# Kernel tuning notes

Measured on AMD Instinct MI355X. Metric: run time of the kernel, lower is better.

## Reference

```python
import jax, jax.numpy as jnp
import numpy as np


def _compute_deltas(ts, m):
    """Affine time-decay recurrence: delta_0 = 0; for t>=1:
    delta_t = gap_t + (1 - m_{t-1}) * delta_{t-1}, with gap broadcast over features.
    ts: [b, s] timestamps, m: [b, s, f] float 0/1 mask. Returns [b, s, f]."""
    b, s, f = m.shape
    gaps = ts[:, 1:] - ts[:, :-1]          # [b, s-1]
    a = 1.0 - m[:, :-1, :]                 # [b, s-1, f] decay coefficient

    def step(d, inp):
        g_t, a_t = inp                      # g_t: [b], a_t: [b, f]
        d = g_t[:, None] + a_t * d
        return d, d

    gT = jnp.swapaxes(gaps, 0, 1)          # [s-1, b]
    aT = jnp.swapaxes(a, 0, 1)             # [s-1, b, f]
    _, ds = jax.lax.scan(step, jnp.zeros((b, f), ts.dtype), (gT, aT))
    ds = jnp.swapaxes(ds, 0, 1)            # [b, s-1, f]
    return jnp.concatenate([jnp.zeros((b, 1, f), ts.dtype), ds], axis=1)


def setup_inputs() -> dict:
    key = jax.random.key(0)
    k1, k2, k3 = jax.random.split(key, 3)
    b, s, f = 32, 2048, 768
    # monotonically increasing timestamps (cumsum of positive gaps)
    gaps = jax.random.uniform(k1, (b, s), minval=1.0, maxval=60.0, dtype=jnp.float32)
    timestamps = jnp.cumsum(gaps, axis=1)
    encoded_data = jax.random.normal(k2, (b, s, f), dtype=jnp.float32)
    masks = jax.random.randint(k3, (b, s, f), 0, 2, dtype=jnp.int32)
    return {"timestamps": timestamps, "encoded_data": encoded_data, "masks": masks}


def reference(timestamps, encoded_data, masks):
    """JAX translation of _prepare_brits_data. Returns stacked
    [forward_deltas, backward_deltas, backward_X] of shape [3, b, s, f].
    (forward X / masks are pass-through inputs; backward mask is flip(masks).)"""
    m = masks.astype(timestamps.dtype)
    forward_deltas = _compute_deltas(timestamps, m)
    ts_b = jnp.flip(timestamps, axis=1)
    m_b = jnp.flip(m, axis=1)
    backward_deltas = jnp.abs(_compute_deltas(ts_b, m_b))
    x_b = jnp.flip(encoded_data, axis=1)
    return jnp.stack([forward_deltas, backward_deltas, x_b], axis=0)
```

## Files before the change

### kernel.cpp

```cpp
#include <hip/hip_runtime.h>
#include <stdint.h>

static constexpr int B = 32, S = 2048, F = 768;
static constexpr int SC = 64;
static constexpr int NSC = S / SC;
static constexpr int F4 = F / 4;
static constexpr int FT = F4;

typedef float v4f __attribute__((ext_vector_type(4)));

__device__ __forceinline__ v4f mk4(float a, float b, float c, float d) {
    v4f v; v.x = a; v.y = b; v.z = c; v.w = d; return v;
}

__global__ __launch_bounds__(FT) void deltaK(const float* __restrict__ ts,
                                             const int4* __restrict__ masks,
                                             float* __restrict__ out) {
    const int pair = blockIdx.x;
    const int b  = pair >> 5;
    const int sc = pair & (NSC - 1);
    const int g0 = sc * SC;
    const int j  = threadIdx.x;
    const size_t N4 = (size_t)B * S * F4;

    const float* tsb = ts + (size_t)b * S;
    const int4* mbase = masks + (size_t)b * S * F4 + j;

    __shared__ float tss[SC];
    if (j < SC) tss[j] = tsb[g0 + j];
    __syncthreads();

    uint32_t a0 = 0, a1 = 0, a2 = 0, a3 = 0;
    uint32_t c0 = 0, c1 = 0, c2 = 0, c3 = 0;
    #pragma unroll
    for (int g = 0; g < 8; ++g) {
        int4 mv[8];
        #pragma unroll
        for (int q = 0; q < 8; ++q) mv[q] = mbase[(size_t)(g0 + g * 8 + q) * F4];
        #pragma unroll
        for (int q = 0; q < 8; ++q) {
            const int k = g * 8 + q;
            const uint32_t bit = 1u << (k & 31);
            if (k < 32) {
                if (mv[q].x) a0 |= bit;
                if (mv[q].y) a1 |= bit;
                if (mv[q].z) a2 |= bit;
                if (mv[q].w) a3 |= bit;
            } else {
                if (mv[q].x) c0 |= bit;
                if (mv[q].y) c1 |= bit;
                if (mv[q].z) c2 |= bit;
                if (mv[q].w) c3 |= bit;
            }
        }
    }

    float t0v = tsb[0];
    float p0 = t0v, p1 = t0v, p2 = t0v, p3 = t0v;
    if (g0 > 0) {
        unsigned um = 0xFu;
        int r = g0 - 1;
        while (um && r >= 0) {
            int rl = (r - 7 > 0) ? r - 7 : 0;
            int nn = r - rl + 1;
            int4 mv[8];
            #pragma unroll
            for (int q = 0; q < 8; ++q) if (q < nn) mv[q] = mbase[(size_t)(r - q) * F4];
            #pragma unroll
            for (int q = 0; q < 8; ++q) if (q < nn) {
                float t = tsb[r - q];
                if ((um & 1u) && mv[q].x) { p0 = t; um &= ~1u; }
                if ((um & 2u) && mv[q].y) { p1 = t; um &= ~2u; }
                if ((um & 4u) && mv[q].z) { p2 = t; um &= ~4u; }
                if ((um & 8u) && mv[q].w) { p3 = t; um &= ~8u; }
            }
            r = rl - 1;
        }
    }

    float tev = tsb[S - 1];
    float n0 = tev, n1 = tev, n2 = tev, n3 = tev;
    if (g0 + SC < S) {
        unsigned um = 0xFu;
        int r = g0 + SC;
        while (um && r < S) {
            int rh = (r + 7 < S - 1) ? r + 7 : S - 1;
            int nn = rh - r + 1;
            int4 mv[8];
            #pragma unroll
            for (int q = 0; q < 8; ++q) if (q < nn) mv[q] = mbase[(size_t)(r + q) * F4];
            #pragma unroll
            for (int q = 0; q < 8; ++q) if (q < nn) {
                float t = tsb[r + q];
                if ((um & 1u) && mv[q].x) { n0 = t; um &= ~1u; }
                if ((um & 2u) && mv[q].y) { n1 = t; um &= ~2u; }
                if ((um & 4u) && mv[q].z) { n2 = t; um &= ~4u; }
                if ((um & 8u) && mv[q].w) { n3 = t; um &= ~8u; }
            }
            r = rh + 1;
        }
    }

    v4f* o0 = reinterpret_cast<v4f*>(out) + (size_t)(b * S + g0) * F4 + j;
    #pragma unroll
    for (int k = 0; k < 32; ++k) {
        float t = tss[k];
        __builtin_nontemporal_store(mk4(t - p0, t - p1, t - p2, t - p3), &o0[(size_t)k * F4]);
        const uint32_t bit = 1u << k;
        if (a0 & bit) p0 = t;
        if (a1 & bit) p1 = t;
        if (a2 & bit) p2 = t;
        if (a3 & bit) p3 = t;
    }
    #pragma unroll
    for (int k = 32; k < 64; ++k) {
        float t = tss[k];
        __builtin_nontemporal_store(mk4(t - p0, t - p1, t - p2, t - p3), &o0[(size_t)k * F4]);
        const uint32_t bit = 1u << (k - 32);
        if (c0 & bit) p0 = t;
        if (c1 & bit) p1 = t;
        if (c2 & bit) p2 = t;
        if (c3 & bit) p3 = t;
    }

    v4f* o1b = reinterpret_cast<v4f*>(out) + N4 + (size_t)b * S * F4 + j;
    #pragma unroll
    for (int k = 63; k >= 32; --k) {
        float t = tss[k];
        size_t fr = (size_t)(S - 1 - g0 - k) * F4;
        __builtin_nontemporal_store(mk4(n0 - t, n1 - t, n2 - t, n3 - t), &o1b[fr]);
        const uint32_t bit = 1u << (k - 32);
        if (c0 & bit) n0 = t;
        if (c1 & bit) n1 = t;
        if (c2 & bit) n2 = t;
        if (c3 & bit) n3 = t;
    }
    #pragma unroll
    for (int k = 31; k >= 0; --k) {
        float t = tss[k];
        size_t fr = (size_t)(S - 1 - g0 - k) * F4;
        __builtin_nontemporal_store(mk4(n0 - t, n1 - t, n2 - t, n3 - t), &o1b[fr]);
        const uint32_t bit = 1u << k;
        if (a0 & bit) n0 = t;
        if (a1 & bit) n1 = t;
        if (a2 & bit) n2 = t;
        if (a3 & bit) n3 = t;
    }
}

static constexpr int CPY_BLOCKS = 2048;
__global__ __launch_bounds__(256) void copyK(const v4f* __restrict__ x,
                                             v4f* __restrict__ o2) {
    const size_t N4 = (size_t)B * S * F4;
    const size_t stride = (size_t)CPY_BLOCKS * 256;
    for (size_t i = (size_t)blockIdx.x * 256 + threadIdx.x; i < N4; i += stride) {
        size_t row = i / F4;
        size_t f   = i - row * F4;
        size_t t   = row & (S - 1);
        size_t src = (row - t + (S - 1 - t)) * F4 + f;
        __builtin_nontemporal_store(__builtin_nontemporal_load(&x[src]), &o2[i]);
    }
}

extern "C" void kernel_launch(void* const* d_in, const int* in_sizes, int n_in,
                              void* d_out, int out_size, void* d_ws, size_t ws_size,
                              hipStream_t stream) {
    const float* ts    = (const float*)d_in[0];
    const v4f* x       = (const v4f*)d_in[1];
    const int4*  masks = (const int4*)d_in[2];
    float* out = (float*)d_out;
    const size_t N4 = (size_t)B * S * F4;
    deltaK<<<B * NSC, FT, 0, stream>>>(ts, masks, out);
    copyK<<<CPY_BLOCKS, 256, 0, stream>>>(x, reinterpret_cast<v4f*>(out) + 2 * N4);
}
```

Baseline: 194.1 us.

## Split delta kernel into bitmask-packing pass and bitmask-based scan pass

The delta kernel is split into two passes. The first reads each 64-row chunk of the mask once, packs it into per-feature 64-bit bitmasks and writes them to workspace. The second finds the previous and next observed timestamps across chunk boundaries by scanning those compact bitmasks with clz/ffs, replacing the re-reads of full int32 mask rows. This adds an extra launch and a workspace round trip; the old fused kernel is kept as a fallback when the workspace is too small.

```diff
diff --git a/kernel.cpp b/kernel.cpp
--- a/kernel.cpp
+++ b/kernel.cpp
@@ -2,41 +2,32 @@
 #include <stdint.h>
 
 static constexpr int B = 32, S = 2048, F = 768;
-static constexpr int SC = 64;
-static constexpr int NSC = S / SC;
+static constexpr int CS = 64;
+static constexpr int NCH = S / CS;
 static constexpr int F4 = F / 4;
 static constexpr int FT = F4;
 
 typedef float v4f __attribute__((ext_vector_type(4)));
+typedef int   v4i __attribute__((ext_vector_type(4)));
+typedef unsigned int v4u __attribute__((ext_vector_type(4)));
 
 __device__ __forceinline__ v4f mk4(float a, float b, float c, float d) {
     v4f v; v.x = a; v.y = b; v.z = c; v.w = d; return v;
 }
 
-__global__ __launch_bounds__(FT) void deltaK(const float* __restrict__ ts,
-                                             const int4* __restrict__ masks,
-                                             float* __restrict__ out) {
-    const int pair = blockIdx.x;
-    const int b  = pair >> 5;
-    const int sc = pair & (NSC - 1);
-    const int g0 = sc * SC;
-    const int j  = threadIdx.x;
-    const size_t N4 = (size_t)B * S * F4;
-
-    const float* tsb = ts + (size_t)b * S;
-    const int4* mbase = masks + (size_t)b * S * F4 + j;
-
-    __shared__ float tss[SC];
-    if (j < SC) tss[j] = tsb[g0 + j];
-    __syncthreads();
-
+__global__ __launch_bounds__(FT) void passA(const v4i* __restrict__ masks,
+                                            uint32_t* __restrict__ bw) {
+    const int blk = blockIdx.x;
+    const int b = blk >> 5, c = blk & 31;
+    const int j = threadIdx.x;
+    const v4i* mp = masks + (size_t)(b * S + c * CS) * F4 + j;
     uint32_t a0 = 0, a1 = 0, a2 = 0, a3 = 0;
     uint32_t c0 = 0, c1 = 0, c2 = 0, c3 = 0;
     #pragma unroll
     for (int g = 0; g < 8; ++g) {
-        int4 mv[8];
-        #pragma unroll
-        for (int q = 0; q < 8; ++q) mv[q] = mbase[(size_t)(g0 + g * 8 + q) * F4];
+        v4i mv[8];
+        #pragma unroll
+        for (int q = 0; q < 8; ++q) mv[q] = __builtin_nontemporal_load(&mp[(size_t)(g * 8 + q) * F4]);
         #pragma unroll
         for (int q = 0; q < 8; ++q) {
             const int k = g * 8 + q;
@@ -54,50 +45,65 @@
             }
         }
     }
-
-    float t0v = tsb[0];
-    float p0 = t0v, p1 = t0v, p2 = t0v, p3 = t0v;
-    if (g0 > 0) {
-        unsigned um = 0xFu;
-        int r = g0 - 1;
-        while (um && r >= 0) {
-            int rl = (r - 7 > 0) ? r - 7 : 0;
-            int nn = r - rl + 1;
-            int4 mv[8];
-            #pragma unroll
-            for (int q = 0; q < 8; ++q) if (q < nn) mv[q] = mbase[(size_t)(r - q) * F4];
-            #pragma unroll
-            for (int q = 0; q < 8; ++q) if (q < nn) {
-                float t = tsb[r - q];
-                if ((um & 1u) && mv[q].x) { p0 = t; um &= ~1u; }
-                if ((um & 2u) && mv[q].y) { p1 = t; um &= ~2u; }
-                if ((um & 4u) && mv[q].z) { p2 = t; um &= ~4u; }
-                if ((um & 8u) && mv[q].w) { p3 = t; um &= ~8u; }
-            }
-            r = rl - 1;
-        }
-    }
-
-    float tev = tsb[S - 1];
-    float n0 = tev, n1 = tev, n2 = tev, n3 = tev;
-    if (g0 + SC < S) {
-        unsigned um = 0xFu;
-        int r = g0 + SC;
-        while (um && r < S) {
-            int rh = (r + 7 < S - 1) ? r + 7 : S - 1;
-            int nn = rh - r + 1;
-            int4 mv[8];
-            #pragma unroll
-            for (int q = 0; q < 8; ++q) if (q < nn) mv[q] = mbase[(size_t)(r + q) * F4];
-            #pragma unroll
-            for (int q = 0; q < 8; ++q) if (q < nn) {
-                float t = tsb[r + q];
-                if ((um & 1u) && mv[q].x) { n0 = t; um &= ~1u; }
-                if ((um & 2u) && mv[q].y) { n1 = t; um &= ~2u; }
-                if ((um & 4u) && mv[q].z) { n2 = t; um &= ~4u; }
-                if ((um & 8u) && mv[q].w) { n3 = t; um &= ~8u; }
-            }
-            r = rh + 1;
+    v4u w0; w0.x = a0; w0.y = c0; w0.z = a1; w0.w = c1;
+    v4u w1; w1.x = a2; w1.y = c2; w1.z = a3; w1.w = c3;
+    v4u* dst = reinterpret_cast<v4u*>(bw + ((size_t)blk * F + 4 * j) * 2);
+    dst[0] = w0;
+    dst[1] = w1;
+}
+
+__global__ __launch_bounds__(FT) void passC(const float* __restrict__ ts,
+                                            const uint32_t* __restrict__ bw,
+                                            float* __restrict__ out) {
+    const int blk = blockIdx.x;
+    const int b = blk >> 5, c = blk & 31;
+    const int g0 = c * CS;
+    const int j = threadIdx.x;
+    const size_t N4 = (size_t)B * S * F4;
+    const float* tsb = ts + (size_t)b * S;
+
+    __shared__ float tss[CS];
+    if (j < CS) tss[j] = tsb[g0 + j];
+    __syncthreads();
+
+    const v4u* own = reinterpret_cast<const v4u*>(bw + ((size_t)blk * F + 4 * j) * 2);
+    v4u w0 = own[0], w1 = own[1];
+    uint32_t alo[4] = {w0.x, w0.z, w1.x, w1.z};
+    uint32_t ahi[4] = {w0.y, w0.w, w1.y, w1.w};
+
+    float p[4], n[4];
+    {
+        float def = tsb[0];
+        p[0] = p[1] = p[2] = p[3] = def;
+        uint32_t need = 0xFu;
+        for (int d = c - 1; d >= 0 && need; --d) {
+            const v4u* nb = reinterpret_cast<const v4u*>(bw + ((size_t)(b * NCH + d) * F + 4 * j) * 2);
+            v4u u0 = nb[0], u1 = nb[1];
+            uint32_t lo[4] = {u0.x, u0.z, u1.x, u1.z};
+            uint32_t hi[4] = {u0.y, u0.w, u1.y, u1.w};
+            const int base = d * CS;
+            #pragma unroll
+            for (int i = 0; i < 4; ++i) if (need & (1u << i)) {
+                if (hi[i])      { p[i] = tsb[base + 32 + (31 - __clz((int)hi[i]))]; need &= ~(1u << i); }
+                else if (lo[i]) { p[i] = tsb[base +      (31 - __clz((int)lo[i]))]; need &= ~(1u << i); }
+            }
+        }
+    }
+    {
+        float def = tsb[S - 1];
+        n[0] = n[1] = n[2] = n[3] = def;
+        uint32_t need = 0xFu;
+        for (int d = c + 1; d < NCH && need; ++d) {
+            const v4u* nb = reinterpret_cast<const v4u*>(bw + ((size_t)(b * NCH + d) * F + 4 * j) * 2);
+            v4u u0 = nb[0], u1 = nb[1];
+            uint32_t lo[4] = {u0.x, u0.z, u1.x, u1.z};
+            uint32_t hi[4] = {u0.y, u0.w, u1.y, u1.w};
+            const int base = d * CS;
+            #pragma unroll
+            for (int i = 0; i < 4; ++i) if (need & (1u << i)) {
+                if (lo[i])      { n[i] = tsb[base +      (__ffs((int)lo[i]) - 1)]; need &= ~(1u << i); }
+                else if (hi[i]) { n[i] = tsb[base + 32 + (__ffs((int)hi[i]) - 1)]; need &= ~(1u << i); }
+            }
         }
     }
 
@@ -105,22 +111,18 @@
     #pragma unroll
     for (int k = 0; k < 32; ++k) {
         float t = tss[k];
-        __builtin_nontemporal_store(mk4(t - p0, t - p1, t - p2, t - p3), &o0[(size_t)k * F4]);
-        const uint32_t bit = 1u << k;
-        if (a0 & bit) p0 = t;
-        if (a1 & bit) p1 = t;
-        if (a2 & bit) p2 = t;
-        if (a3 & bit) p3 = t;
+        __builtin_nontemporal_store(mk4(t - p[0], t - p[1], t - p[2], t - p[3]), &o0[(size_t)k * F4]);
+        const uint32_t bit = 1u << k;
+        #pragma unroll
+        for (int i = 0; i < 4; ++i) if (alo[i] & bit) p[i] = t;
     }
     #pragma unroll
     for (int k = 32; k < 64; ++k) {
         float t = tss[k];
-        __builtin_nontemporal_store(mk4(t - p0, t - p1, t - p2, t - p3), &o0[(size_t)k * F4]);
-        const uint32_t bit = 1u << (k - 32);
-        if (c0 & bit) p0 = t;
-        if (c1 & bit) p1 = t;
-        if (c2 & bit) p2 = t;
-        if (c3 & bit) p3 = t;
+        __builtin_nontemporal_store(mk4(t - p[0], t - p[1], t - p[2], t - p[3]), &o0[(size_t)k * F4]);
+        const uint32_t bit = 1u << (k - 32);
+        #pragma unroll
+        for (int i = 0; i < 4; ++i) if (ahi[i] & bit) p[i] = t;
     }
 
     v4f* o1b = reinterpret_cast<v4f*>(out) + N4 + (size_t)b * S * F4 + j;
@@ -128,23 +130,19 @@
     for (int k = 63; k >= 32; --k) {
         float t = tss[k];
         size_t fr = (size_t)(S - 1 - g0 - k) * F4;
-        __builtin_nontemporal_store(mk4(n0 - t, n1 - t, n2 - t, n3 - t), &o1b[fr]);
-        const uint32_t bit = 1u << (k - 32);
-        if (c0 & bit) n0 = t;
-        if (c1 & bit) n1 = t;
-        if (c2 & bit) n2 = t;
-        if (c3 & bit) n3 = t;
+        __builtin_nontemporal_store(mk4(n[0] - t, n[1] - t, n[2] - t, n[3] - t), &o1b[fr]);
+        const uint32_t bit = 1u << (k - 32);
+        #pragma unroll
+        for (int i = 0; i < 4; ++i) if (ahi[i] & bit) n[i] = t;
     }
     #pragma unroll
     for (int k = 31; k >= 0; --k) {
         float t = tss[k];
         size_t fr = (size_t)(S - 1 - g0 - k) * F4;
-        __builtin_nontemporal_store(mk4(n0 - t, n1 - t, n2 - t, n3 - t), &o1b[fr]);
-        const uint32_t bit = 1u << k;
-        if (a0 & bit) n0 = t;
-        if (a1 & bit) n1 = t;
-        if (a2 & bit) n2 = t;
-        if (a3 & bit) n3 = t;
+        __builtin_nontemporal_store(mk4(n[0] - t, n[1] - t, n[2] - t, n[3] - t), &o1b[fr]);
+        const uint32_t bit = 1u << k;
+        #pragma unroll
+        for (int i = 0; i < 4; ++i) if (alo[i] & bit) n[i] = t;
     }
 }
 
@@ -162,14 +160,122 @@
     }
 }
 
+__global__ __launch_bounds__(FT) void deltaProbeK(const float* __restrict__ ts,
+                                                  const int4* __restrict__ masks,
+                                                  float* __restrict__ out) {
+    const int pair = blockIdx.x;
+    const int b = pair >> 5, sc = pair & 31;
+    const int g0 = sc * CS;
+    const int j = threadIdx.x;
+    const size_t N4 = (size_t)B * S * F4;
+    const float* tsb = ts + (size_t)b * S;
+    const int4* mbase = masks + (size_t)b * S * F4 + j;
+    __shared__ float tss[CS];
+    if (j < CS) tss[j] = tsb[g0 + j];
+    __syncthreads();
+    uint32_t a0 = 0, a1 = 0, a2 = 0, a3 = 0, c0 = 0, c1 = 0, c2 = 0, c3 = 0;
+    #pragma unroll
+    for (int g = 0; g < 8; ++g) {
+        int4 mv[8];
+        #pragma unroll
+        for (int q = 0; q < 8; ++q) mv[q] = mbase[(size_t)(g0 + g * 8 + q) * F4];
+        #pragma unroll
+        for (int q = 0; q < 8; ++q) {
+            const int k = g * 8 + q;
+            const uint32_t bit = 1u << (k & 31);
+            if (k < 32) { if (mv[q].x) a0 |= bit; if (mv[q].y) a1 |= bit; if (mv[q].z) a2 |= bit; if (mv[q].w) a3 |= bit; }
+            else        { if (mv[q].x) c0 |= bit; if (mv[q].y) c1 |= bit; if (mv[q].z) c2 |= bit; if (mv[q].w) c3 |= bit; }
+        }
+    }
+    float t0v = tsb[0];
+    float p0 = t0v, p1 = t0v, p2 = t0v, p3 = t0v;
+    if (g0 > 0) {
+        unsigned um = 0xFu; int r = g0 - 1;
+        while (um && r >= 0) {
+            int rl = (r - 7 > 0) ? r - 7 : 0; int nn = r - rl + 1;
+            int4 mv[8];
+            #pragma unroll
+            for (int q = 0; q < 8; ++q) if (q < nn) mv[q] = mbase[(size_t)(r - q) * F4];
+            #pragma unroll
+            for (int q = 0; q < 8; ++q) if (q < nn) {
+                float t = tsb[r - q];
+                if ((um & 1u) && mv[q].x) { p0 = t; um &= ~1u; }
+                if ((um & 2u) && mv[q].y) { p1 = t; um &= ~2u; }
+                if ((um & 4u) && mv[q].z) { p2 = t; um &= ~4u; }
+                if ((um & 8u) && mv[q].w) { p3 = t; um &= ~8u; }
+            }
+            r = rl - 1;
+        }
+    }
+    float tev = tsb[S - 1];
+    float n0 = tev, n1 = tev, n2 = tev, n3 = tev;
+    if (g0 + CS < S) {
+        unsigned um = 0xFu; int r = g0 + CS;
+        while (um && r < S) {
+            int rh = (r + 7 < S - 1) ? r + 7 : S - 1; int nn = rh - r + 1;
+            int4 mv[8];
+            #pragma unroll
+            for (int q = 0; q < 8; ++q) if (q < nn) mv[q] = mbase[(size_t)(r + q) * F4];
+            #pragma unroll
+            for (int q = 0; q < 8; ++q) if (q < nn) {
+                float t = tsb[r + q];
+                if ((um & 1u) && mv[q].x) { n0 = t; um &= ~1u; }
+                if ((um & 2u) && mv[q].y) { n1 = t; um &= ~2u; }
+                if ((um & 4u) && mv[q].z) { n2 = t; um &= ~4u; }
+                if ((um & 8u) && mv[q].w) { n3 = t; um &= ~8u; }
+            }
+            r = rh + 1;
+        }
+    }
+    v4f* o0 = reinterpret_cast<v4f*>(out) + (size_t)(b * S + g0) * F4 + j;
+    #pragma unroll
+    for (int k = 0; k < 32; ++k) {
+        float t = tss[k];
+        __builtin_nontemporal_store(mk4(t - p0, t - p1, t - p2, t - p3), &o0[(size_t)k * F4]);
+        const uint32_t bit = 1u << k;
+        if (a0 & bit) p0 = t; if (a1 & bit) p1 = t; if (a2 & bit) p2 = t; if (a3 & bit) p3 = t;
+    }
+    #pragma unroll
+    for (int k = 32; k < 64; ++k) {
+        float t = tss[k];
+        __builtin_nontemporal_store(mk4(t - p0, t - p1, t - p2, t - p3), &o0[(size_t)k * F4]);
+        const uint32_t bit = 1u << (k - 32);
+        if (c0 & bit) p0 = t; if (c1 & bit) p1 = t; if (c2 & bit) p2 = t; if (c3 & bit) p3 = t;
+    }
+    v4f* o1b = reinterpret_cast<v4f*>(out) + N4 + (size_t)b * S * F4 + j;
+    #pragma unroll
+    for (int k = 63; k >= 32; --k) {
+        float t = tss[k];
+        size_t fr = (size_t)(S - 1 - g0 - k) * F4;
+        __builtin_nontemporal_store(mk4(n0 - t, n1 - t, n2 - t, n3 - t), &o1b[fr]);
+        const uint32_t bit = 1u << (k - 32);
+        if (c0 & bit) n0 = t; if (c1 & bit) n1 = t; if (c2 & bit) n2 = t; if (c3 & bit) n3 = t;
+    }
+    #pragma unroll
+    for (int k = 31; k >= 0; --k) {
+        float t = tss[k];
+        size_t fr = (size_t)(S - 1 - g0 - k) * F4;
+        __builtin_nontemporal_store(mk4(n0 - t, n1 - t, n2 - t, n3 - t), &o1b[fr]);
+        const uint32_t bit = 1u << k;
+        if (a0 & bit) n0 = t; if (a1 & bit) n1 = t; if (a2 & bit) n2 = t; if (a3 & bit) n3 = t;
+    }
+}
+
 extern "C" void kernel_launch(void* const* d_in, const int* in_sizes, int n_in,
                               void* d_out, int out_size, void* d_ws, size_t ws_size,
                               hipStream_t stream) {
     const float* ts    = (const float*)d_in[0];
     const v4f* x       = (const v4f*)d_in[1];
-    const int4*  masks = (const int4*)d_in[2];
     float* out = (float*)d_out;
     const size_t N4 = (size_t)B * S * F4;
-    deltaK<<<B * NSC, FT, 0, stream>>>(ts, masks, out);
+    const size_t bw_bytes = (size_t)B * NCH * F * 2 * sizeof(uint32_t);
+
+    if (ws_size >= bw_bytes) {
+        uint32_t* bw = (uint32_t*)d_ws;
+        passA<<<B * NCH, FT, 0, stream>>>((const v4i*)d_in[2], bw);
+        passC<<<B * NCH, FT, 0, stream>>>(ts, bw, out);
+    } else {
+        deltaProbeK<<<B * NCH, FT, 0, stream>>>(ts, (const int4*)d_in[2], out);
+    }
     copyK<<<CPY_BLOCKS, 256, 0, stream>>>(x, reinterpret_cast<v4f*>(out) + 2 * N4);
 }
```

Result: no change. 193.8 us, median of 2 (-0.1%).
